# Kernel optimization log

Measured on AMD Instinct MI355X. Metric: run time of the kernel, lower is better.

## Reference

```python
import jax, jax.numpy as jnp
import numpy as np

D_MODEL = 1024
N_HEADS = 16
HEAD_DIM = D_MODEL // N_HEADS
THETA = 10000.0
B, S = 4, 2048


def setup_inputs() -> dict:
    key = jax.random.key(0)
    ks = jax.random.split(key, 5)
    scale = 1.0 / np.sqrt(D_MODEL)
    x = jax.random.normal(ks[0], (B, S, D_MODEL), dtype=jnp.float32)
    token_positions = jnp.broadcast_to(jnp.arange(S, dtype=jnp.int32)[None, :], (B, S))
    WQ = jax.random.normal(ks[1], (D_MODEL, D_MODEL), dtype=jnp.float32) * scale
    WK = jax.random.normal(ks[2], (D_MODEL, D_MODEL), dtype=jnp.float32) * scale
    WV = jax.random.normal(ks[3], (D_MODEL, D_MODEL), dtype=jnp.float32) * scale
    WO = jax.random.normal(ks[4], (D_MODEL, D_MODEL), dtype=jnp.float32) * scale
    return {"x": x, "token_positions": token_positions, "WQ": WQ, "WK": WK, "WV": WV, "WO": WO}


def _apply_rope(t, token_positions):
    # t: [b, h, s, d]; token_positions: [b, s]
    d = t.shape[-1]
    inv_freq = THETA ** (-jnp.arange(0, d, 2, dtype=jnp.float32) / d)  # [d/2]
    ang = token_positions.astype(jnp.float32)[:, None, :, None] * inv_freq  # [b,1,s,d/2]
    cos, sin = jnp.cos(ang), jnp.sin(ang)
    t_even, t_odd = t[..., 0::2], t[..., 1::2]
    r_even = t_even * cos - t_odd * sin
    r_odd = t_even * sin + t_odd * cos
    out = jnp.stack([r_even, r_odd], axis=-1)  # interleave pairs back
    return out.reshape(t.shape)


def reference(x, token_positions, WQ, WK, WV, WO):
    b, s, _ = x.shape
    def proj(W):
        y = jnp.einsum('bsd,ed->bse', x, W)  # Linear: x @ W^T, W is [out,in]
        return y.reshape(b, s, N_HEADS, HEAD_DIM).transpose(0, 2, 1, 3)  # [b,h,s,d]
    Q = _apply_rope(proj(WQ), token_positions)
    K = _apply_rope(proj(WK), token_positions)
    V = proj(WV)
    scores = jnp.einsum('bhqd,bhkd->bhqk', Q, K) / jnp.sqrt(jnp.float32(HEAD_DIM))
    causal = jnp.tril(jnp.ones((s, s), dtype=bool))
    scores = jnp.where(causal, scores, -jnp.inf)
    attn = jax.nn.softmax(scores, axis=-1)
    out = jnp.einsum('bhqk,bhkd->bhqd', attn, V)
    out = out.transpose(0, 2, 1, 3).reshape(b, s, D_MODEL)
    return jnp.einsum('bse,oe->bso', out, WO)
```

## Files before the change

### kernel.cpp

```cpp
#include <hip/hip_runtime.h>

typedef __bf16 bf16x8 __attribute__((ext_vector_type(8)));
typedef __bf16 bf16x2 __attribute__((ext_vector_type(2)));
typedef float f32x4 __attribute__((ext_vector_type(4)));
typedef float f32x2 __attribute__((ext_vector_type(2)));
typedef unsigned short u16;
typedef unsigned int u32;

#define MFMA16(a, b, c) __builtin_amdgcn_mfma_f32_16x16x32_bf16((a), (b), (c), 0, 0, 0)

__device__ __forceinline__ u16 f2b(float f) {
  u32 u = __float_as_uint(f);
  u += 0x7FFFu + ((u >> 16) & 1u);
  return (u16)(u >> 16);
}
__device__ __forceinline__ float b2f(u16 h) { return __uint_as_float(((u32)h) << 16); }

__device__ __forceinline__ u32 pkbf(float a, float b) {
  bf16x2 h = {(__bf16)a, (__bf16)b};
  return __builtin_bit_cast(u32, h);
}

__device__ __forceinline__ float max3f(float a, float b, float c) {
  float d;
  asm("v_max3_f32 %0, %1, %2, %3" : "=v"(d) : "v"(a), "v"(b), "v"(c));
  return d;
}

__device__ __forceinline__ float exp2_(float x) {
#if __has_builtin(__builtin_amdgcn_exp2f)
  return __builtin_amdgcn_exp2f(x);
#else
  return exp2f(x);
#endif
}

__device__ __forceinline__ void glds16(const void* g, void* l) {
  __builtin_amdgcn_global_load_lds((const __attribute__((address_space(1))) void*)g,
                                   (__attribute__((address_space(3))) void*)l, 16, 0, 0);
}

__global__ __launch_bounds__(256) void cvt_k(const float* __restrict__ x,
                                             const float* __restrict__ wq,
                                             const float* __restrict__ wk,
                                             const float* __restrict__ wv,
                                             const float* __restrict__ wo,
                                             u16* __restrict__ dst) {
  size_t e = ((size_t)blockIdx.x * 256 + threadIdx.x) * 4;
  const float* src;
  size_t off;
  if (e < 8388608ull) {
    src = x; off = e;
  } else {
    size_t r = e - 8388608ull;
    u32 wi = (u32)(r >> 20);
    off = r & 1048575ull;
    src = (wi == 0) ? wq : (wi == 1) ? wk : (wi == 2) ? wv : wo;
  }
  float4 v = *(const float4*)(src + off);
  ushort4 o = make_ushort4(f2b(v.x), f2b(v.y), f2b(v.z), f2b(v.w));
  *(ushort4*)(dst + e) = o;
}

__global__ __launch_bounds__(256) void rope_tab_k(const int* __restrict__ pos,
                                                  float2* __restrict__ tab) {
  int i = blockIdx.x * 256 + threadIdx.x;
  int row = i >> 5, j = i & 31;
  float p = (float)pos[row];
  float inv = exp2f((float)j * -0.41524101186092029f);
  float s, c;
  sincosf(p * inv, &s, &c);
  tab[i] = make_float2(c, s);
}

__global__ __launch_bounds__(256, 3) void gemm_qkv_k(const u16* __restrict__ Xb,
                                                     const u16* __restrict__ Wq,
                                                     const u16* __restrict__ Wk,
                                                     const u16* __restrict__ Wv,
                                                     const float2* __restrict__ tab,
                                                     u16* __restrict__ Qp,
                                                     u16* __restrict__ Kp,
                                                     u16* __restrict__ Vt) {
  __shared__ u16 As[3][4096];
  __shared__ u16 Bs[3][4096];
  const int wgid = blockIdx.x;
  const int xcd = wgid & 7;
  const int idx = wgid >> 3;
  const int P = xcd * 24 + (idx >> 3);
  const int nt = idx & 7;
  const int z = P >> 6;
  const int mt = P & 63;
  const u16* W = (z == 0) ? Wq : (z == 1) ? Wk : Wv;
  const int t = threadIdx.x;
  const int wave = t >> 6, lane = t & 63;
  const int lr = lane & 15, lg = lane >> 4;
  const int wr = wave >> 1, wc = wave & 1;

  const int rr0 = t >> 3;
  const int s8 = t & 7;
  const int sl8 = s8 ^ (rr0 & 7);
  const int js = sl8 >> 2;
  const int kcs = sl8 & 3;
  const u16* aS = Xb + (size_t)(mt * 128 + rr0 + 64 * js) * 1024 + kcs * 8;
  const u16* bS = W + (size_t)(nt * 128 + rr0 + 64 * js) * 1024 + kcs * 8;

  f32x4 acc[4][4];
#pragma unroll
  for (int i = 0; i < 4; ++i)
#pragma unroll
    for (int j = 0; j < 4; ++j) acc[i][j] = (f32x4){0.f, 0.f, 0.f, 0.f};

#pragma unroll
  for (int tt = 0; tt < 2; ++tt) {
    const int kcol = tt * 32;
    glds16(aS + kcol, &As[tt][t * 8]);
    glds16(aS + 32 * 1024 + kcol, &As[tt][2048 + t * 8]);
    glds16(bS + kcol, &Bs[tt][t * 8]);
    glds16(bS + 32 * 1024 + kcol, &Bs[tt][2048 + t * 8]);
  }
  asm volatile("s_waitcnt vmcnt(4)" ::: "memory");
  __builtin_amdgcn_s_barrier();

  const int arb = lr * 64 + (((wr << 2) + lg) ^ (lr & 7)) * 8;
  const int brb = lr * 64 + (((wc << 2) + lg) ^ (lr & 7)) * 8;

  int sl = 0, sp2 = 2;
  for (int tau = 0; tau < 32; ++tau) {
    const u16* Asl = &As[sl][0];
    const u16* Bsl = &Bs[sl][0];
    bf16x8 af[4], bf[4];
#pragma unroll
    for (int mi = 0; mi < 4; ++mi) af[mi] = *(const bf16x8*)&Asl[arb + mi * 1024];
#pragma unroll
    for (int nj = 0; nj < 4; ++nj) bf[nj] = *(const bf16x8*)&Bsl[brb + nj * 1024];
    if (tau < 30) {
      u16* Ad = &As[sp2][0];
      u16* Bd = &Bs[sp2][0];
      const int kcol = (tau + 2) * 32;
      glds16(aS + kcol, &Ad[t * 8]);
      glds16(aS + 32 * 1024 + kcol, &Ad[2048 + t * 8]);
      glds16(bS + kcol, &Bd[t * 8]);
      glds16(bS + 32 * 1024 + kcol, &Bd[2048 + t * 8]);
    }
    asm volatile("s_waitcnt lgkmcnt(0)" ::: "memory");
    __builtin_amdgcn_sched_barrier(0);
    __builtin_amdgcn_s_setprio(1);
#pragma unroll
    for (int mi = 0; mi < 4; ++mi)
#pragma unroll
      for (int nj = 0; nj < 4; ++nj)
        acc[mi][nj] = MFMA16(af[mi], bf[nj], acc[mi][nj]);
    __builtin_amdgcn_s_setprio(0);
    __builtin_amdgcn_sched_barrier(0);
    if (tau < 30) asm volatile("s_waitcnt vmcnt(4)" ::: "memory");
    else asm volatile("s_waitcnt vmcnt(0)" ::: "memory");
    __builtin_amdgcn_s_barrier();
    sl = (sl == 2) ? 0 : sl + 1;
    sp2 = (sp2 == 2) ? 0 : sp2 + 1;
  }

  const int rbase = mt * 128 + wr * 64 + lg * 4;
  const int cbase = nt * 128 + wc * 64 + lr;
  if (z < 2) {
    u16* out = (z == 0) ? Qp : Kp;
    const float scl = (z == 0) ? 0.18033688011112043f : 1.0f;
#pragma unroll
    for (int mi = 0; mi < 4; ++mi)
#pragma unroll
      for (int nj = 0; nj < 4; ++nj) {
        int row0 = rbase + mi * 16;
        int col = cbase + nj * 16;
        int j = (col >> 1) & 31;
        float sgn = (col & 1) ? 1.f : -1.f;
#pragma unroll
        for (int r = 0; r < 4; ++r) {
          float self = acc[mi][nj][r];
          float partner = __shfl_xor(self, 1);
          float2 cs = tab[(size_t)(row0 + r) * 32 + j];
          float o = (self * cs.x + partner * cs.y * sgn) * scl;
          out[(size_t)(row0 + r) * 1024 + col] = f2b(o);
        }
      }
  } else {
#pragma unroll
    for (int mi = 0; mi < 4; ++mi)
#pragma unroll
      for (int nj = 0; nj < 4; ++nj) {
        int row0 = rbase + mi * 16;
        int e = cbase + nj * 16;
        int b = row0 >> 11, s = row0 & 2047;
        ushort4 pk = make_ushort4(f2b(acc[mi][nj][0]), f2b(acc[mi][nj][1]),
                                  f2b(acc[mi][nj][2]), f2b(acc[mi][nj][3]));
        *(ushort4*)&Vt[((size_t)(b * 1024 + e)) * 2048 + s] = pk;
      }
  }
}

__global__ __launch_bounds__(512, 4) void fattn_k(const u16* __restrict__ Qp,
                                                  const u16* __restrict__ Kp,
                                                  const u16* __restrict__ Vt,
                                                  u16* __restrict__ Ao) {
  __shared__ u16 Ks[2][64 * 64];
  __shared__ u16 Vs[2][64 * 64];
  __shared__ u16 Ps[8][16 * 64];
  const int blk = blockIdx.x;
  const int g = blk & 7, jj = blk >> 3;
  const int bh = g * 8 + (jj & 7);
  const int J = jj >> 3;
  const int qt = (J < 4) ? (7 - J) : (J - 4);
  const int b = bh >> 4, h = bh & 15;
  const int tid = threadIdx.x, wave = tid >> 6, lane = tid & 63;
  const int lr = lane & 15, lg = lane >> 4;
  const int q0w = qt * 256 + wave * 32;

  bf16x8 qf[2][2];
#pragma unroll
  for (int qh = 0; qh < 2; ++qh) {
    const u16* qb = Qp + ((size_t)(b * 2048 + q0w + qh * 16 + lr)) * 1024 + h * 64 + lg * 8;
    qf[qh][0] = *(const bf16x8*)qb;
    qf[qh][1] = *(const bf16x8*)(qb + 32);
  }

  float m[2], l[2];
  f32x4 oacc[2][4];
#pragma unroll
  for (int qh = 0; qh < 2; ++qh) {
    m[qh] = -1e30f; l[qh] = 0.f;
#pragma unroll
    for (int d4 = 0; d4 < 4; ++d4) oacc[qh][d4] = (f32x4){0.f, 0.f, 0.f, 0.f};
  }
  const f32x4 fz = {0.f, 0.f, 0.f, 0.f};

  const int srow = lane >> 3;
  const int schunk = (lane & 7) ^ srow;
  const u16* kbase = Kp + ((size_t)(b * 2048 + 8 * wave + srow)) * 1024 + h * 64 + schunk * 8;
  const u16* vbase = Vt + ((size_t)(b * 1024 + h * 64 + 8 * wave + srow)) * 2048 + schunk * 8;
  char* psbase = (char*)&Ps[wave][0];

  const int ktmax = 4 * qt + 3;
  const int ktneed = 4 * qt + (wave >> 1);

  glds16(kbase, &Ks[0][(8 * wave) * 64]);
  glds16(vbase, &Vs[0][(8 * wave) * 64]);

  int cur = 0;
  for (int kt = 0; kt <= ktmax; ++kt, cur ^= 1) {
    __syncthreads();
    if (kt < ktmax) {
      const int nx = cur ^ 1, k1 = kt + 1;
      glds16(kbase + (size_t)k1 * 65536, &Ks[nx][(8 * wave) * 64]);
      glds16(vbase + k1 * 64, &Vs[nx][(8 * wave) * 64]);
    }
    if (kt > ktneed) continue;
    const u16* KB = &Ks[cur][0];
    const u16* VB = &Vs[cur][0];

    f32x4 sc[2][4];
#pragma unroll
    for (int ks = 0; ks < 4; ++ks) {
      const int krow = ks * 16 + lr;
      const int swk = lr & 7;
      bf16x8 kf0 = *(const bf16x8*)&KB[krow * 64 + ((lg ^ swk) * 8)];
      bf16x8 kf1 = *(const bf16x8*)&KB[krow * 64 + (((lg + 4) ^ swk) * 8)];
#pragma unroll
      for (int qh = 0; qh < 2; ++qh) {
        f32x4 s = MFMA16(kf0, qf[qh][0], fz);
        s = MFMA16(kf1, qf[qh][1], s);
        sc[qh][ks] = s;
      }
    }
    if (kt == ktneed) {
#pragma unroll
      for (int qh = 0; qh < 2; ++qh) {
        int q = q0w + qh * 16 + lr;
#pragma unroll
        for (int ks = 0; ks < 4; ++ks)
#pragma unroll
          for (int r = 0; r < 4; ++r) {
            int kv = kt * 64 + ks * 16 + lg * 4 + r;
            if (kv > q) sc[qh][ks][r] = -__builtin_inff();
          }
      }
    }

#pragma unroll
    for (int qh = 0; qh < 2; ++qh) {
      float t0 = max3f(sc[qh][0][0], sc[qh][0][1], sc[qh][0][2]);
      float t1 = max3f(sc[qh][0][3], sc[qh][1][0], sc[qh][1][1]);
      float t2 = max3f(sc[qh][1][2], sc[qh][1][3], sc[qh][2][0]);
      float t3 = max3f(sc[qh][2][1], sc[qh][2][2], sc[qh][2][3]);
      float t4 = max3f(sc[qh][3][0], sc[qh][3][1], sc[qh][3][2]);
      float pm = max3f(max3f(t0, t1, t2), max3f(t3, t4, sc[qh][3][3]),
                       -1e30f);
      pm = fmaxf(pm, __shfl_xor(pm, 16));
      pm = fmaxf(pm, __shfl_xor(pm, 32));
      if (__any(pm > m[qh] + 8.f)) {
        float mn = fmaxf(m[qh], pm);
        float corr = exp2_(m[qh] - mn);
        m[qh] = mn;
        l[qh] *= corr;
        float cb[4];
#pragma unroll
        for (int r = 0; r < 4; ++r) cb[r] = __shfl(corr, (lane & 48) | (lg * 4 + r));
#pragma unroll
        for (int d4 = 0; d4 < 4; ++d4)
#pragma unroll
          for (int r = 0; r < 4; ++r) oacc[qh][d4][r] *= cb[r];
      }
      const f32x2 ms = {m[qh], m[qh]};
      f32x2 rs2 = {0.f, 0.f};
#pragma unroll
      for (int ks = 0; ks < 4; ++ks) {
        f32x2 lo = {sc[qh][ks][0], sc[qh][ks][1]};
        f32x2 hi = {sc[qh][ks][2], sc[qh][ks][3]};
        lo = lo - ms;
        hi = hi - ms;
        lo[0] = exp2_(lo[0]); lo[1] = exp2_(lo[1]);
        hi[0] = exp2_(hi[0]); hi[1] = exp2_(hi[1]);
        rs2 += lo;
        rs2 += hi;
        sc[qh][ks][0] = lo[0]; sc[qh][ks][1] = lo[1];
        sc[qh][ks][2] = hi[0]; sc[qh][ks][3] = hi[1];
      }
      float rs = rs2[0] + rs2[1];
      rs += __shfl_xor(rs, 16);
      rs += __shfl_xor(rs, 32);
      l[qh] += rs;
    }

    bf16x8 pa[2][2];
#pragma unroll
    for (int qh = 0; qh < 2; ++qh) {
      const int swp = lr & 7;
#pragma unroll
      for (int ks = 0; ks < 4; ++ks) {
        const int chunk = (2 * ks + (lg >> 1)) ^ swp;
        char* p = psbase + lr * 128 + chunk * 16 + (lg & 1) * 8;
        *(uint2*)p = make_uint2(pkbf(sc[qh][ks][0], sc[qh][ks][1]),
                                pkbf(sc[qh][ks][2], sc[qh][ks][3]));
      }
      pa[qh][0] = *(const bf16x8*)(psbase + lr * 128 + ((lg ^ swp) * 16));
      pa[qh][1] = *(const bf16x8*)(psbase + lr * 128 + (((lg + 4) ^ swp) * 16));
    }
#pragma unroll
    for (int d4 = 0; d4 < 4; ++d4) {
      const int vrow = d4 * 16 + lr;
      const int swv = lr & 7;
      bf16x8 vf0 = *(const bf16x8*)&VB[vrow * 64 + ((lg ^ swv) * 8)];
      bf16x8 vf1 = *(const bf16x8*)&VB[vrow * 64 + (((lg + 4) ^ swv) * 8)];
      oacc[0][d4] = MFMA16(pa[0][0], vf0, oacc[0][d4]);
      oacc[0][d4] = MFMA16(pa[0][1], vf1, oacc[0][d4]);
      oacc[1][d4] = MFMA16(pa[1][0], vf0, oacc[1][d4]);
      oacc[1][d4] = MFMA16(pa[1][1], vf1, oacc[1][d4]);
    }
  }

#pragma unroll
  for (int qh = 0; qh < 2; ++qh) {
    float lb[4];
#pragma unroll
    for (int r = 0; r < 4; ++r) lb[r] = __shfl(l[qh], (lane & 48) | (lg * 4 + r));
#pragma unroll
    for (int r = 0; r < 4; ++r) {
      float inv = 1.f / lb[r];
      int q = q0w + qh * 16 + lg * 4 + r;
      u16* orow = Ao + ((size_t)(b * 2048 + q)) * 1024 + h * 64 + lr;
#pragma unroll
      for (int d4 = 0; d4 < 4; ++d4) orow[d4 * 16] = f2b(oacc[qh][d4][r] * inv);
    }
  }
}

__global__ __launch_bounds__(512, 2) void gemm_wo_k(const u16* __restrict__ Ab,
                                                    const u16* __restrict__ Wo,
                                                    float* __restrict__ Out) {
  __shared__ u16 As[3][16384];
  __shared__ u16 Bs[3][8192];
  const int wgid = blockIdx.x;
  const int xcd = wgid & 7;
  const int idx = wgid >> 3;
  const int mt = xcd * 4 + (idx >> 3);
  const int nt = idx & 7;
  const int t = threadIdx.x;
  const int wave = t >> 6, lane = t & 63;
  const int lr = lane & 15, lg = lane >> 4;
  const int wr = wave >> 1, wc = wave & 1;

  const int srow = t >> 3;
  const int scc = t & 7;
  const int ssw = scc ^ (srow & 7);
  const u16* aA = Ab + (size_t)(mt * 256 + srow) * 1024 + ssw * 8;
  const u16* bB = Wo + (size_t)(nt * 128 + srow) * 1024 + ssw * 8;

  f32x4 acc[4][4];
#pragma unroll
  for (int i = 0; i < 4; ++i)
#pragma unroll
    for (int j = 0; j < 4; ++j) acc[i][j] = (f32x4){0.f, 0.f, 0.f, 0.f};

#pragma unroll
  for (int tt = 0; tt < 2; ++tt) {
    const int kt = tt * 64;
    glds16(aA + kt, &As[tt][t * 8]);
    glds16(aA + 64 * 1024 + kt, &As[tt][4096 + t * 8]);
    glds16(bB + kt, &Bs[tt][t * 8]);
    glds16(aA + 128 * 1024 + kt, &As[tt][8192 + t * 8]);
    glds16(aA + 192 * 1024 + kt, &As[tt][12288 + t * 8]);
    glds16(bB + 64 * 1024 + kt, &Bs[tt][4096 + t * 8]);
  }
  asm volatile("s_waitcnt vmcnt(6)" ::: "memory");
  __builtin_amdgcn_s_barrier();

  const int arow = (wr * 64 + lr) * 64;
  const int brow = (wc * 64 + lr) * 64;
  const int sw = lr & 7;

  int sl = 0;
  for (int tau = 0; tau < 16; ++tau) {
    const int sp2 = (sl + 2 >= 3) ? sl - 1 : sl + 2;
    const u16* Asl = &As[sl][0];
    const u16* Bsl = &Bs[sl][0];
    u16* Ad = &As[sp2][0];
    u16* Bd = &Bs[sp2][0];
    const int kt2 = (tau + 2) * 64;
    bf16x8 af[4], bf[4];

    {
      const int koff = (lg ^ sw) * 8;
#pragma unroll
      for (int mi = 0; mi < 4; ++mi)
        af[mi] = *(const bf16x8*)&Asl[arow + mi * 1024 + koff];
#pragma unroll
      for (int nj = 0; nj < 4; ++nj)
        bf[nj] = *(const bf16x8*)&Bsl[brow + nj * 1024 + koff];
    }
    if (tau < 14) {
      glds16(aA + kt2, &Ad[t * 8]);
      glds16(aA + 64 * 1024 + kt2, &Ad[4096 + t * 8]);
      glds16(bB + kt2, &Bd[t * 8]);
    }
    __builtin_amdgcn_s_barrier();
    asm volatile("s_waitcnt lgkmcnt(0)" ::: "memory");
    __builtin_amdgcn_sched_barrier(0);
    __builtin_amdgcn_s_setprio(1);
#pragma unroll
    for (int mi = 0; mi < 4; ++mi)
#pragma unroll
      for (int nj = 0; nj < 4; ++nj)
        acc[mi][nj] = MFMA16(af[mi], bf[nj], acc[mi][nj]);
    __builtin_amdgcn_s_setprio(0);
    __builtin_amdgcn_sched_barrier(0);
    __builtin_amdgcn_s_barrier();

    {
      const int koff = ((4 + lg) ^ sw) * 8;
#pragma unroll
      for (int mi = 0; mi < 4; ++mi)
        af[mi] = *(const bf16x8*)&Asl[arow + mi * 1024 + koff];
#pragma unroll
      for (int nj = 0; nj < 4; ++nj)
        bf[nj] = *(const bf16x8*)&Bsl[brow + nj * 1024 + koff];
    }
    if (tau < 14) {
      glds16(aA + 128 * 1024 + kt2, &Ad[8192 + t * 8]);
      glds16(aA + 192 * 1024 + kt2, &Ad[12288 + t * 8]);
      glds16(bB + 64 * 1024 + kt2, &Bd[4096 + t * 8]);
    }
    __builtin_amdgcn_s_barrier();
    asm volatile("s_waitcnt lgkmcnt(0)" ::: "memory");
    __builtin_amdgcn_sched_barrier(0);
    __builtin_amdgcn_s_setprio(1);
#pragma unroll
    for (int mi = 0; mi < 4; ++mi)
#pragma unroll
      for (int nj = 0; nj < 4; ++nj)
        acc[mi][nj] = MFMA16(af[mi], bf[nj], acc[mi][nj]);
    __builtin_amdgcn_s_setprio(0);
    __builtin_amdgcn_sched_barrier(0);
    if (tau < 14) asm volatile("s_waitcnt vmcnt(6)" ::: "memory");
    else asm volatile("s_waitcnt vmcnt(0)" ::: "memory");
    __builtin_amdgcn_s_barrier();
    sl = (sl == 2) ? 0 : sl + 1;
  }

  const int rbase = mt * 256 + wr * 64 + lg * 4;
  const int cbase = nt * 128 + wc * 64 + lr;
#pragma unroll
  for (int mi = 0; mi < 4; ++mi)
#pragma unroll
    for (int nj = 0; nj < 4; ++nj) {
      int row0 = rbase + mi * 16;
      int col = cbase + nj * 16;
#pragma unroll
      for (int r = 0; r < 4; ++r)
        Out[(size_t)(row0 + r) * 1024 + col] = acc[mi][nj][r];
    }
}

extern "C" void kernel_launch(void* const* d_in, const int* in_sizes, int n_in,
                              void* d_out, int out_size, void* d_ws, size_t ws_size,
                              hipStream_t stream) {
  const float* x = (const float*)d_in[0];
  const int* pos = (const int*)d_in[1];
  const float* wq = (const float*)d_in[2];
  const float* wk = (const float*)d_in[3];
  const float* wv = (const float*)d_in[4];
  const float* wo = (const float*)d_in[5];

  char* ws = (char*)d_ws;
  u16* xb = (u16*)ws;
  u16* wqb = xb + 8388608;
  u16* wkb = wqb + 1048576;
  u16* wvb = wkb + 1048576;
  u16* wob = wvb + 1048576;
  float2* tab = (float2*)(ws + 25165824);
  u16* Qp = (u16*)(ws + 27262976);
  u16* Kp = (u16*)(ws + 27262976 + 16777216);
  u16* Vt = (u16*)(ws + 27262976 + 2 * 16777216);
  u16* Ao = (u16*)(ws + 27262976 + 3 * 16777216);

  hipLaunchKernelGGL(cvt_k, dim3(12288), dim3(256), 0, stream, x, wq, wk, wv, wo, xb);
  hipLaunchKernelGGL(rope_tab_k, dim3(1024), dim3(256), 0, stream, pos, tab);
  hipLaunchKernelGGL(gemm_qkv_k, dim3(1536), dim3(256), 0, stream, xb, wqb, wkb, wvb,
                     tab, Qp, Kp, Vt);
  hipLaunchKernelGGL(fattn_k, dim3(512), dim3(512), 0, stream, Qp, Kp, Vt, Ao);
  hipLaunchKernelGGL(gemm_wo_k, dim3(256), dim3(512), 0, stream, Ao, wob, (float*)d_out);
}
```

Before: 172.9 us.

## Halve attention query tile to 128 rows, doubling block count

Each flash-attention wave now handles 16 query rows instead of 32, so a block covers 128 queries and the grid doubles to 1024 blocks. The query-tile ordering changes to a simple longest-first schedule, and launch bounds are raised to allow more resident blocks. This is meant to improve load balance across the causal triangle and raise occupancy. The cost is that each K/V tile loaded into LDS is reused by half as many queries, doubling K/V global traffic and the number of barriers per unit of work.

```diff
diff --git a/kernel.cpp b/kernel.cpp
--- a/kernel.cpp
+++ b/kernel.cpp
@@ -196,7 +196,7 @@
   }
 }
 
-__global__ __launch_bounds__(512, 4) void fattn_k(const u16* __restrict__ Qp,
+__global__ __launch_bounds__(512, 6) void fattn_k(const u16* __restrict__ Qp,
                                                   const u16* __restrict__ Kp,
                                                   const u16* __restrict__ Vt,
                                                   u16* __restrict__ Ao) {
@@ -206,29 +206,23 @@
   const int blk = blockIdx.x;
   const int g = blk & 7, jj = blk >> 3;
   const int bh = g * 8 + (jj & 7);
-  const int J = jj >> 3;
-  const int qt = (J < 4) ? (7 - J) : (J - 4);
+  const int qt = 15 - (jj >> 3);
   const int b = bh >> 4, h = bh & 15;
   const int tid = threadIdx.x, wave = tid >> 6, lane = tid & 63;
   const int lr = lane & 15, lg = lane >> 4;
-  const int q0w = qt * 256 + wave * 32;
-
-  bf16x8 qf[2][2];
-#pragma unroll
-  for (int qh = 0; qh < 2; ++qh) {
-    const u16* qb = Qp + ((size_t)(b * 2048 + q0w + qh * 16 + lr)) * 1024 + h * 64 + lg * 8;
-    qf[qh][0] = *(const bf16x8*)qb;
-    qf[qh][1] = *(const bf16x8*)(qb + 32);
-  }
-
-  float m[2], l[2];
-  f32x4 oacc[2][4];
-#pragma unroll
-  for (int qh = 0; qh < 2; ++qh) {
-    m[qh] = -1e30f; l[qh] = 0.f;
-#pragma unroll
-    for (int d4 = 0; d4 < 4; ++d4) oacc[qh][d4] = (f32x4){0.f, 0.f, 0.f, 0.f};
-  }
+  const int q0w = qt * 128 + wave * 16;
+
+  bf16x8 qf0, qf1;
+  {
+    const u16* qb = Qp + ((size_t)(b * 2048 + q0w + lr)) * 1024 + h * 64 + lg * 8;
+    qf0 = *(const bf16x8*)qb;
+    qf1 = *(const bf16x8*)(qb + 32);
+  }
+
+  float m = -1e30f, l = 0.f;
+  f32x4 oacc[4];
+#pragma unroll
+  for (int d4 = 0; d4 < 4; ++d4) oacc[d4] = (f32x4){0.f, 0.f, 0.f, 0.f};
   const f32x4 fz = {0.f, 0.f, 0.f, 0.f};
 
   const int srow = lane >> 3;
@@ -237,8 +231,8 @@
   const u16* vbase = Vt + ((size_t)(b * 1024 + h * 64 + 8 * wave + srow)) * 2048 + schunk * 8;
   char* psbase = (char*)&Ps[wave][0];
 
-  const int ktmax = 4 * qt + 3;
-  const int ktneed = 4 * qt + (wave >> 1);
+  const int ktmax = 2 * qt + 1;
+  const int ktneed = 2 * qt + (wave >> 2);
 
   glds16(kbase, &Ks[0][(8 * wave) * 64]);
   glds16(vbase, &Vs[0][(8 * wave) * 64]);
@@ -255,92 +249,83 @@
     const u16* KB = &Ks[cur][0];
     const u16* VB = &Vs[cur][0];
 
-    f32x4 sc[2][4];
+    f32x4 sc[4];
 #pragma unroll
     for (int ks = 0; ks < 4; ++ks) {
       const int krow = ks * 16 + lr;
       const int swk = lr & 7;
       bf16x8 kf0 = *(const bf16x8*)&KB[krow * 64 + ((lg ^ swk) * 8)];
       bf16x8 kf1 = *(const bf16x8*)&KB[krow * 64 + (((lg + 4) ^ swk) * 8)];
-#pragma unroll
-      for (int qh = 0; qh < 2; ++qh) {
-        f32x4 s = MFMA16(kf0, qf[qh][0], fz);
-        s = MFMA16(kf1, qf[qh][1], s);
-        sc[qh][ks] = s;
-      }
+      f32x4 s = MFMA16(kf0, qf0, fz);
+      s = MFMA16(kf1, qf1, s);
+      sc[ks] = s;
     }
     if (kt == ktneed) {
-#pragma unroll
-      for (int qh = 0; qh < 2; ++qh) {
-        int q = q0w + qh * 16 + lr;
-#pragma unroll
-        for (int ks = 0; ks < 4; ++ks)
-#pragma unroll
-          for (int r = 0; r < 4; ++r) {
-            int kv = kt * 64 + ks * 16 + lg * 4 + r;
-            if (kv > q) sc[qh][ks][r] = -__builtin_inff();
-          }
-      }
-    }
-
-#pragma unroll
-    for (int qh = 0; qh < 2; ++qh) {
-      float t0 = max3f(sc[qh][0][0], sc[qh][0][1], sc[qh][0][2]);
-      float t1 = max3f(sc[qh][0][3], sc[qh][1][0], sc[qh][1][1]);
-      float t2 = max3f(sc[qh][1][2], sc[qh][1][3], sc[qh][2][0]);
-      float t3 = max3f(sc[qh][2][1], sc[qh][2][2], sc[qh][2][3]);
-      float t4 = max3f(sc[qh][3][0], sc[qh][3][1], sc[qh][3][2]);
-      float pm = max3f(max3f(t0, t1, t2), max3f(t3, t4, sc[qh][3][3]),
-                       -1e30f);
+      int q = q0w + lr;
+#pragma unroll
+      for (int ks = 0; ks < 4; ++ks)
+#pragma unroll
+        for (int r = 0; r < 4; ++r) {
+          int kv = kt * 64 + ks * 16 + lg * 4 + r;
+          if (kv > q) sc[ks][r] = -__builtin_inff();
+        }
+    }
+
+    {
+      float t0 = max3f(sc[0][0], sc[0][1], sc[0][2]);
+      float t1 = max3f(sc[0][3], sc[1][0], sc[1][1]);
+      float t2 = max3f(sc[1][2], sc[1][3], sc[2][0]);
+      float t3 = max3f(sc[2][1], sc[2][2], sc[2][3]);
+      float t4 = max3f(sc[3][0], sc[3][1], sc[3][2]);
+      float pm = max3f(max3f(t0, t1, t2), max3f(t3, t4, sc[3][3]), -1e30f);
       pm = fmaxf(pm, __shfl_xor(pm, 16));
       pm = fmaxf(pm, __shfl_xor(pm, 32));
-      if (__any(pm > m[qh] + 8.f)) {
-        float mn = fmaxf(m[qh], pm);
-        float corr = exp2_(m[qh] - mn);
-        m[qh] = mn;
-        l[qh] *= corr;
+      if (__any(pm > m + 8.f)) {
+        float mn = fmaxf(m, pm);
+        float corr = exp2_(m - mn);
+        m = mn;
+        l *= corr;
         float cb[4];
 #pragma unroll
         for (int r = 0; r < 4; ++r) cb[r] = __shfl(corr, (lane & 48) | (lg * 4 + r));
 #pragma unroll
         for (int d4 = 0; d4 < 4; ++d4)
 #pragma unroll
-          for (int r = 0; r < 4; ++r) oacc[qh][d4][r] *= cb[r];
+          for (int r = 0; r < 4; ++r) oacc[d4][r] *= cb[r];
       }
-      const f32x2 ms = {m[qh], m[qh]};
+      const f32x2 ms = {m, m};
       f32x2 rs2 = {0.f, 0.f};
 #pragma unroll
       for (int ks = 0; ks < 4; ++ks) {
-        f32x2 lo = {sc[qh][ks][0], sc[qh][ks][1]};
-        f32x2 hi = {sc[qh][ks][2], sc[qh][ks][3]};
+        f32x2 lo = {sc[ks][0], sc[ks][1]};
+        f32x2 hi = {sc[ks][2], sc[ks][3]};
         lo = lo - ms;
         hi = hi - ms;
         lo[0] = exp2_(lo[0]); lo[1] = exp2_(lo[1]);
         hi[0] = exp2_(hi[0]); hi[1] = exp2_(hi[1]);
         rs2 += lo;
         rs2 += hi;
-        sc[qh][ks][0] = lo[0]; sc[qh][ks][1] = lo[1];
-        sc[qh][ks][2] = hi[0]; sc[qh][ks][3] = hi[1];
+        sc[ks][0] = lo[0]; sc[ks][1] = lo[1];
+        sc[ks][2] = hi[0]; sc[ks][3] = hi[1];
       }
       float rs = rs2[0] + rs2[1];
       rs += __shfl_xor(rs, 16);
       rs += __shfl_xor(rs, 32);
-      l[qh] += rs;
-    }
-
-    bf16x8 pa[2][2];
-#pragma unroll
-    for (int qh = 0; qh < 2; ++qh) {
+      l += rs;
+    }
+
+    bf16x8 pa0, pa1;
+    {
       const int swp = lr & 7;
 #pragma unroll
       for (int ks = 0; ks < 4; ++ks) {
         const int chunk = (2 * ks + (lg >> 1)) ^ swp;
         char* p = psbase + lr * 128 + chunk * 16 + (lg & 1) * 8;
-        *(uint2*)p = make_uint2(pkbf(sc[qh][ks][0], sc[qh][ks][1]),
-                                pkbf(sc[qh][ks][2], sc[qh][ks][3]));
+        *(uint2*)p = make_uint2(pkbf(sc[ks][0], sc[ks][1]),
+                                pkbf(sc[ks][2], sc[ks][3]));
       }
-      pa[qh][0] = *(const bf16x8*)(psbase + lr * 128 + ((lg ^ swp) * 16));
-      pa[qh][1] = *(const bf16x8*)(psbase + lr * 128 + (((lg + 4) ^ swp) * 16));
+      pa0 = *(const bf16x8*)(psbase + lr * 128 + ((lg ^ swp) * 16));
+      pa1 = *(const bf16x8*)(psbase + lr * 128 + (((lg + 4) ^ swp) * 16));
     }
 #pragma unroll
     for (int d4 = 0; d4 < 4; ++d4) {
@@ -348,25 +333,22 @@
       const int swv = lr & 7;
       bf16x8 vf0 = *(const bf16x8*)&VB[vrow * 64 + ((lg ^ swv) * 8)];
       bf16x8 vf1 = *(const bf16x8*)&VB[vrow * 64 + (((lg + 4) ^ swv) * 8)];
-      oacc[0][d4] = MFMA16(pa[0][0], vf0, oacc[0][d4]);
-      oacc[0][d4] = MFMA16(pa[0][1], vf1, oacc[0][d4]);
-      oacc[1][d4] = MFMA16(pa[1][0], vf0, oacc[1][d4]);
-      oacc[1][d4] = MFMA16(pa[1][1], vf1, oacc[1][d4]);
-    }
-  }
-
-#pragma unroll
-  for (int qh = 0; qh < 2; ++qh) {
+      oacc[d4] = MFMA16(pa0, vf0, oacc[d4]);
+      oacc[d4] = MFMA16(pa1, vf1, oacc[d4]);
+    }
+  }
+
+  {
     float lb[4];
 #pragma unroll
-    for (int r = 0; r < 4; ++r) lb[r] = __shfl(l[qh], (lane & 48) | (lg * 4 + r));
+    for (int r = 0; r < 4; ++r) lb[r] = __shfl(l, (lane & 48) | (lg * 4 + r));
 #pragma unroll
     for (int r = 0; r < 4; ++r) {
       float inv = 1.f / lb[r];
-      int q = q0w + qh * 16 + lg * 4 + r;
+      int q = q0w + lg * 4 + r;
       u16* orow = Ao + ((size_t)(b * 2048 + q)) * 1024 + h * 64 + lr;
 #pragma unroll
-      for (int d4 = 0; d4 < 4; ++d4) orow[d4 * 16] = f2b(oacc[qh][d4][r] * inv);
+      for (int d4 = 0; d4 < 4; ++d4) orow[d4 * 16] = f2b(oacc[d4][r] * inv);
     }
   }
 }
@@ -523,6 +505,6 @@
   hipLaunchKernelGGL(rope_tab_k, dim3(1024), dim3(256), 0, stream, pos, tab);
   hipLaunchKernelGGL(gemm_qkv_k, dim3(1536), dim3(256), 0, stream, xb, wqb, wkb, wvb,
                      tab, Qp, Kp, Vt);
-  hipLaunchKernelGGL(fattn_k, dim3(512), dim3(512), 0, stream, Qp, Kp, Vt, Ao);
+  hipLaunchKernelGGL(fattn_k, dim3(1024), dim3(512), 0, stream, Qp, Kp, Vt, Ao);
   hipLaunchKernelGGL(gemm_wo_k, dim3(256), dim3(512), 0, stream, Ao, wob, (float*)d_out);
 }
```

New measurement: 162.7 us. -5.9%, faster.
